# Performance work log

Hardware: AMD Instinct MI355X
Metric: run time of the kernel (lower is better)

The kernel has to match this reference:

```python
import jax, jax.numpy as jnp
import numpy as np

DIM = 768
HEADS = 8
EPS = 1e-6


def _layernorm(x, gamma, beta):
    # torch: mean over last dim; std with Bessel correction (unbiased, ddof=1)
    mean = jnp.mean(x, axis=-1, keepdims=True)
    std = jnp.std(x, axis=-1, keepdims=True, ddof=1)
    return gamma * (x - mean) / (std + EPS) + beta


def setup_inputs() -> dict:
    key = jax.random.key(0)
    ks = jax.random.split(key, 8)
    s = 0.02
    return {
        "x": jax.random.normal(ks[0], (16384, DIM), dtype=jnp.float32),
        "wq_w": jax.random.normal(ks[1], (DIM, DIM), dtype=jnp.float32) * s,
        "wq_b": jnp.zeros((DIM,), dtype=jnp.float32),
        "wk_w": jax.random.normal(ks[2], (DIM, DIM), dtype=jnp.float32) * s,
        "wk_b": jnp.zeros((DIM,), dtype=jnp.float32),
        "wv_w": jax.random.normal(ks[3], (DIM, DIM), dtype=jnp.float32) * s,
        "wv_b": jnp.zeros((DIM,), dtype=jnp.float32),
        "d1_w": jax.random.normal(ks[4], (4 * DIM, DIM), dtype=jnp.float32) * s,
        "d1_b": jnp.zeros((4 * DIM,), dtype=jnp.float32),
        "d2_w": jax.random.normal(ks[5], (DIM, 4 * DIM), dtype=jnp.float32) * s,
        "d2_b": jnp.zeros((DIM,), dtype=jnp.float32),
        "g1": jnp.ones((1,), dtype=jnp.float32),
        "b1": jnp.zeros((1,), dtype=jnp.float32),
        "g2": jnp.ones((1,), dtype=jnp.float32),
        "b2": jnp.zeros((1,), dtype=jnp.float32),
    }


def reference(x, wq_w, wq_b, wk_w, wk_b, wv_w, wv_b,
              d1_w, d1_b, d2_w, d2_b, g1, b1, g2, b2):
    T = x.shape[0]
    # --- pre-LN + attention ---
    xn = _layernorm(x, g1, b1)                      # [T, D]
    q = xn @ wq_w.T + wq_b                          # [T, D]
    k = xn @ wk_w.T + wk_b
    v = xn @ wv_w.T + wv_b
    # faithful to q.view(-1, num_heads, key_dim): groups of HEADS tokens
    q = q.reshape(T // HEADS, HEADS, DIM)
    k = k.reshape(T // HEADS, HEADS, DIM)
    v = v.reshape(T // HEADS, HEADS, DIM)
    scores = jnp.einsum('ghd,gkd->ghk', q, k) / jnp.sqrt(jnp.float32(DIM))
    attn_w = jax.nn.softmax(scores, axis=-1)        # [T/8, 8, 8]
    attn = jnp.einsum('ghk,gkd->ghd', attn_w, v).reshape(T, DIM)
    x = attn + x
    # --- pre-LN + MLP ---
    xn = _layernorm(x, g2, b2)
    h = jax.nn.gelu(xn @ d1_w.T + d1_b, approximate=False)  # [T, 4D]
    x = (h @ d2_w.T + d2_b) + x
    return x
```

## Files before the change

### kernel.cpp

```cpp
#include <hip/hip_runtime.h>
#include <stdint.h>

#define DIM 768
#define HDIM 3072

typedef unsigned short u16;
typedef unsigned char u8;
typedef unsigned int u32;
typedef __bf16 bf16x8 __attribute__((ext_vector_type(8)));
typedef float f32x2 __attribute__((ext_vector_type(2)));
typedef float f32x4 __attribute__((ext_vector_type(4)));
typedef float f32x16 __attribute__((ext_vector_type(16)));
typedef int i32x8 __attribute__((ext_vector_type(8)));

__device__ __forceinline__ u16 f2b(float f) {
    union { float f; unsigned i; } v; v.f = f;
    unsigned r = (v.i + 0x7FFFu + ((v.i >> 16) & 1u)) >> 16;
    return (u16)r;
}
__device__ __forceinline__ unsigned pack2b(float a, float b) {
    return (unsigned)f2b(a) | ((unsigned)f2b(b) << 16);
}
__device__ __forceinline__ float gelu_f(float v) {
    float u = v * (1.5957691216f + 0.07135481627f * v * v);
    float e = __builtin_amdgcn_exp2f(-1.442695041f * u);
    return v * __builtin_amdgcn_rcpf(1.0f + e);
}
__device__ __forceinline__ void gl_lds16(const void* g, void* l) {
    __builtin_amdgcn_global_load_lds(
        (__attribute__((address_space(1))) void*)(g),
        (__attribute__((address_space(3))) void*)(l), 16, 0, 0);
}

__global__ __launch_bounds__(256) void cvt_bf16(const float4* __restrict__ s,
                                                ushort4* __restrict__ d, int n4) {
    int i = blockIdx.x * 256 + threadIdx.x;
    if (i < n4) {
        float4 v = s[i];
        ushort4 o;
        o.x = f2b(v.x); o.y = f2b(v.y); o.z = f2b(v.z); o.w = f2b(v.w);
        d[i] = o;
    }
}

__global__ __launch_bounds__(256) void cvt_fp8(const float4* __restrict__ s,
                                               unsigned* __restrict__ d, int n4) {
    int i = blockIdx.x * 256 + threadIdx.x;
    if (i < n4) {
        float4 v = s[i];
        int p = __builtin_amdgcn_cvt_pk_fp8_f32(v.x, v.y, 0, false);
        p = __builtin_amdgcn_cvt_pk_fp8_f32(v.z, v.w, p, true);
        d[i] = (unsigned)p;
    }
}

__global__ void pack_bias3(const float* __restrict__ a, const float* __restrict__ b,
                           const float* __restrict__ c, float* __restrict__ o) {
    int i = blockIdx.x * 256 + threadIdx.x;
    if (i < DIM) { o[i] = a[i]; o[i + DIM] = b[i]; o[i + 2 * DIM] = c[i]; }
}

__global__ __launch_bounds__(256) void ln_rows_f8(const float* __restrict__ x, u8* __restrict__ xn,
                                                  const float* __restrict__ g, const float* __restrict__ b) {
    int row = blockIdx.x * 4 + (threadIdx.x >> 6);
    int lane = threadIdx.x & 63;
    const float* xr = x + (size_t)row * DIM + lane * 12;
    float v[12];
#pragma unroll
    for (int i = 0; i < 3; ++i) {
        float4 t = ((const float4*)xr)[i];
        v[i * 4 + 0] = t.x; v[i * 4 + 1] = t.y; v[i * 4 + 2] = t.z; v[i * 4 + 3] = t.w;
    }
    float s = 0.f, ss = 0.f;
#pragma unroll
    for (int i = 0; i < 12; ++i) { s += v[i]; ss += v[i] * v[i]; }
#pragma unroll
    for (int o = 32; o; o >>= 1) { s += __shfl_xor(s, o); ss += __shfl_xor(ss, o); }
    float mean = s * (1.f / DIM);
    float var = (ss - (float)DIM * mean * mean) * (1.f / (DIM - 1));
    float denom = sqrtf(var) + 1e-6f;
    float sc = g[0] / denom, bb = b[0] - mean * sc;
    unsigned* outp = (unsigned*)(xn + (size_t)row * DIM + lane * 12);
#pragma unroll
    for (int i = 0; i < 3; ++i) {
        int p = __builtin_amdgcn_cvt_pk_fp8_f32(v[i * 4 + 0] * sc + bb, v[i * 4 + 1] * sc + bb, 0, false);
        p = __builtin_amdgcn_cvt_pk_fp8_f32(v[i * 4 + 2] * sc + bb, v[i * 4 + 3] * sc + bb, p, true);
        outp[i] = (unsigned)p;
    }
}

template <int EPI, int N, int K>
__global__ __launch_bounds__(256)
void gemm_f8(const u8* __restrict__ A, const u8* __restrict__ B,
             const float* __restrict__ bias, const float* __restrict__ resid,
             u8* __restrict__ Co, float* __restrict__ Cf) {
    __shared__ __align__(16) u8 smem[32768];
    u8* As = smem;
    u8* Bs = smem + 16384;
    const int tid = threadIdx.x, lane = tid & 63, wave = tid >> 6;
    const int row0 = blockIdx.x * 128, col0 = blockIdx.y * 128;
    const int wm = (wave >> 1) * 64, wn = (wave & 1) * 64;
    f32x16 acc[2][2] = {};

    const int srow = lane >> 3;
    const int schunk = ((lane & 7) ^ srow) * 16;
    const u8* Ag = A + (size_t)(row0 + wave * 8 + srow) * K + schunk;
    const u8* Bg = B + (size_t)(col0 + wave * 8 + srow) * K + schunk;
    const size_t s32 = (size_t)32 * K;
    u8* AsW = As + wave * 1024;
    u8* BsW = Bs + wave * 1024;

    const int r31 = lane & 31, khalf = lane >> 5;

    for (int kb = 0; kb < K; kb += 128) {
#pragma unroll
        for (int i = 0; i < 4; ++i) {
            gl_lds16(Ag + i * s32, AsW + i * 4096);
            gl_lds16(Bg + i * s32, BsW + i * 4096);
        }
        Ag += 128; Bg += 128;
        __syncthreads();
#pragma unroll
        for (int ks = 0; ks < 2; ++ks) {
            const int c0 = ks * 4 + khalf * 2;
            union { i32x8 v; uint4 q[2]; } af[2], bfr[2];
#pragma unroll
            for (int ib = 0; ib < 2; ++ib) {
                const int r = wm + ib * 32 + r31;
                const u8* base = As + r * 128;
                const int x7 = (r & 7);
                af[ib].q[0] = *(const uint4*)(base + ((c0 ^ x7) * 16));
                af[ib].q[1] = *(const uint4*)(base + (((c0 + 1) ^ x7) * 16));
            }
#pragma unroll
            for (int jb = 0; jb < 2; ++jb) {
                const int r = wn + jb * 32 + r31;
                const u8* base = Bs + r * 128;
                const int x7 = (r & 7);
                bfr[jb].q[0] = *(const uint4*)(base + ((c0 ^ x7) * 16));
                bfr[jb].q[1] = *(const uint4*)(base + (((c0 + 1) ^ x7) * 16));
            }
#pragma unroll
            for (int ib = 0; ib < 2; ++ib)
#pragma unroll
                for (int jb = 0; jb < 2; ++jb)
                    acc[ib][jb] = __builtin_amdgcn_mfma_scale_f32_32x32x64_f8f6f4(
                        bfr[jb].v, af[ib].v, acc[ib][jb], 0, 0,
                        0, 0x7F7F7F7F, 0, 0x7F7F7F7F);
        }
        __syncthreads();
    }
    if (EPI == 0) {
        u32* Cs = (u32*)smem;
#pragma unroll
        for (int ib = 0; ib < 2; ++ib) {
            const int row = wm + ib * 32 + r31;
            const int rx = row & 31;
#pragma unroll
            for (int jb = 0; jb < 2; ++jb)
#pragma unroll
                for (int gq = 0; gq < 4; ++gq) {
                    const int cb = wn + jb * 32 + gq * 8 + 4 * khalf;
                    float4 bv = *(const float4*)(bias + col0 + cb);
                    float v0 = acc[ib][jb][gq * 4 + 0] + bv.x;
                    float v1 = acc[ib][jb][gq * 4 + 1] + bv.y;
                    float v2 = acc[ib][jb][gq * 4 + 2] + bv.z;
                    float v3 = acc[ib][jb][gq * 4 + 3] + bv.w;
                    int p = __builtin_amdgcn_cvt_pk_fp8_f32(v0, v1, 0, false);
                    p = __builtin_amdgcn_cvt_pk_fp8_f32(v2, v3, p, true);
                    Cs[row * 32 + ((cb >> 2) ^ rx)] = (u32)p;
                }
        }
        __syncthreads();
#pragma unroll
        for (int pr = 0; pr < 4; ++pr) {
            const int r = pr * 32 + (tid >> 3);
            const int rx = r & 31;
            const int dwb = (tid & 7) * 4;
            uint4 o;
            o.x = Cs[r * 32 + ((dwb + 0) ^ rx)];
            o.y = Cs[r * 32 + ((dwb + 1) ^ rx)];
            o.z = Cs[r * 32 + ((dwb + 2) ^ rx)];
            o.w = Cs[r * 32 + ((dwb + 3) ^ rx)];
            *(uint4*)(Co + (size_t)(row0 + r) * N + col0 + dwb * 4) = o;
        }
    } else {
        float* Cs = (float*)smem;
#pragma unroll
        for (int pass = 0; pass < 2; ++pass) {
            const int ss = (wm >> 1) + r31;
            const int sx = ss & 7;
#pragma unroll
            for (int jb = 0; jb < 2; ++jb)
#pragma unroll
                for (int gq = 0; gq < 4; ++gq) {
                    const int cb = wn + jb * 32 + gq * 8 + 4 * khalf;
                    float4 bv = *(const float4*)(bias + col0 + cb);
                    float4 v;
                    v.x = acc[pass][jb][gq * 4 + 0] + bv.x;
                    v.y = acc[pass][jb][gq * 4 + 1] + bv.y;
                    v.z = acc[pass][jb][gq * 4 + 2] + bv.z;
                    v.w = acc[pass][jb][gq * 4 + 3] + bv.w;
                    *(float4*)(Cs + ss * 128 + (((cb >> 2) ^ sx) << 2)) = v;
                }
            __syncthreads();
            const int s = tid >> 2;
            const int grow = row0 + (s >> 5) * 64 + pass * 32 + (s & 31);
#pragma unroll
            for (int k = 0; k < 8; ++k) {
                const int c = k * 4 + (tid & 3);
                float4 v = *(const float4*)(Cs + s * 128 + ((c ^ (s & 7)) << 2));
                const size_t gi = (size_t)grow * N + col0 + c * 4;
                float4 rv = *(const float4*)(resid + gi);
                v.x += rv.x; v.y += rv.y; v.z += rv.z; v.w += rv.w;
                *(float4*)(Cf + gi) = v;
            }
            if (pass == 0) __syncthreads();
        }
    }
}

template <int N, int K>
__global__ __launch_bounds__(256)
void gemm_up(const u16* __restrict__ A, const u16* __restrict__ B,
             const float* __restrict__ bias, u8* __restrict__ C8) {
    __shared__ __align__(16) u16 As[128 * 64];
    __shared__ __align__(16) u16 Bs[128 * 64];
    const int tid = threadIdx.x;
    const int row0 = blockIdx.x * 128, col0 = blockIdx.y * 128;
    const int lane = tid & 63, wave = tid >> 6;
    const int wm = (wave >> 1) * 64, wn = (wave & 1) * 64;
    const int la = lane & 15, qd = lane >> 4;
    f32x4 acc[4][4] = {};

    const int srow = lane >> 3;
    const int schunk = (lane & 7) ^ srow;
    const u16* Ag = A + (size_t)(row0 + wave * 8 + srow) * K + schunk * 8;
    const u16* Bg = B + (size_t)(col0 + wave * 8 + srow) * K + schunk * 8;
    const size_t s32 = (size_t)32 * K;
    u16* AsW = &As[wave * 512];
    u16* BsW = &Bs[wave * 512];
    const int x7 = la & 7;

    for (int kb = 0; kb < K; kb += 64) {
#pragma unroll
        for (int i = 0; i < 4; ++i) {
            gl_lds16(Ag + i * s32, AsW + i * 2048);
            gl_lds16(Bg + i * s32, BsW + i * 2048);
        }
        Ag += 64; Bg += 64;
        __syncthreads();
#pragma unroll
        for (int ks = 0; ks < 2; ++ks) {
            const int cp = ((ks * 4 + qd) ^ x7) * 8;
            bf16x8 af[4], bfr[4];
#pragma unroll
            for (int i = 0; i < 4; ++i)
                af[i] = *(const bf16x8*)(&As[(wm + i * 16 + la) * 64 + cp]);
#pragma unroll
            for (int j = 0; j < 4; ++j)
                bfr[j] = *(const bf16x8*)(&Bs[(wn + j * 16 + la) * 64 + cp]);
#pragma unroll
            for (int i = 0; i < 4; ++i)
#pragma unroll
                for (int j = 0; j < 4; ++j)
                    acc[i][j] = __builtin_amdgcn_mfma_f32_16x16x32_bf16(bfr[j], af[i], acc[i][j], 0, 0, 0);
        }
        __syncthreads();
    }
    u32* Cs = (u32*)As;
#pragma unroll
    for (int i = 0; i < 4; ++i) {
        const int row = wm + i * 16 + la;
        const int rx = row & 31;
#pragma unroll
        for (int j = 0; j < 4; ++j) {
            const int cb = wn + j * 16 + qd * 4;
            float4 bv = *(const float4*)(bias + col0 + cb);
            float v0 = gelu_f(acc[i][j][0] + bv.x);
            float v1 = gelu_f(acc[i][j][1] + bv.y);
            float v2 = gelu_f(acc[i][j][2] + bv.z);
            float v3 = gelu_f(acc[i][j][3] + bv.w);
            int p = __builtin_amdgcn_cvt_pk_fp8_f32(v0, v1, 0, false);
            p = __builtin_amdgcn_cvt_pk_fp8_f32(v2, v3, p, true);
            Cs[row * 32 + ((cb >> 2) ^ rx)] = (u32)p;
        }
    }
    __syncthreads();
#pragma unroll
    for (int pr = 0; pr < 4; ++pr) {
        const int r = pr * 32 + (tid >> 3);
        const int rx = r & 31;
        const int dwb = (tid & 7) * 4;
        uint4 o;
        o.x = Cs[r * 32 + ((dwb + 0) ^ rx)];
        o.y = Cs[r * 32 + ((dwb + 1) ^ rx)];
        o.z = Cs[r * 32 + ((dwb + 2) ^ rx)];
        o.w = Cs[r * 32 + ((dwb + 3) ^ rx)];
        *(uint4*)(C8 + (size_t)(row0 + r) * N + col0 + dwb * 4) = o;
    }
}

__global__ __launch_bounds__(256)
void attn_ln(const u8* __restrict__ qkv, const float* __restrict__ x,
             float* __restrict__ x1, u16* __restrict__ xn2,
             const float* __restrict__ g, const float* __restrict__ b) {
    __shared__ __align__(16) u8 sq[8 * 2304];
    __shared__ float sw[64];
    const int tid = threadIdx.x;
    const uint4* src = (const uint4*)(qkv + (size_t)blockIdx.x * (8 * 2304));
    uint4* dst = (uint4*)sq;
#pragma unroll
    for (int i = 0; i < 5; ++i) {
        int idx = tid + i * 256;
        if (idx < 1152) dst[idx] = src[idx];
    }
    __syncthreads();
    const u32* sq32 = (const u32*)sq;
    const int wave = tid >> 6, lane = tid & 63;
#pragma unroll 2
    for (int p = wave * 16; p < wave * 16 + 16; ++p) {
        const u32* qr = sq32 + (p >> 3) * 576 + lane * 3;
        const u32* kr = sq32 + (p & 7) * 576 + 192 + lane * 3;
        float s = 0.f;
#pragma unroll
        for (int i = 0; i < 3; ++i) {
            u32 qd = qr[i], kd = kr[i];
            f32x2 q0 = __builtin_amdgcn_cvt_pk_f32_fp8(qd, false);
            f32x2 q1 = __builtin_amdgcn_cvt_pk_f32_fp8(qd, true);
            f32x2 k0 = __builtin_amdgcn_cvt_pk_f32_fp8(kd, false);
            f32x2 k1 = __builtin_amdgcn_cvt_pk_f32_fp8(kd, true);
            s += q0[0] * k0[0] + q0[1] * k0[1] + q1[0] * k1[0] + q1[1] * k1[1];
        }
#pragma unroll
        for (int o = 32; o; o >>= 1) s += __shfl_xor(s, o);
        if (lane == 0) sw[p] = s;
    }
    __syncthreads();
    if (tid < 8) {
        const float scl = 0.03608439182435161f;
        float e[8]; float m = -1e30f;
#pragma unroll
        for (int j = 0; j < 8; ++j) m = fmaxf(m, sw[tid * 8 + j]);
        float sum = 0.f;
#pragma unroll
        for (int j = 0; j < 8; ++j) { e[j] = expf((sw[tid * 8 + j] - m) * scl); sum += e[j]; }
        float inv = 1.f / sum;
#pragma unroll
        for (int j = 0; j < 8; ++j) sw[tid * 8 + j] = e[j] * inv;
    }
    __syncthreads();
    const int h = tid >> 5, li = tid & 31;
    float w[8];
#pragma unroll
    for (int kk = 0; kk < 8; ++kk) w[kk] = sw[h * 8 + kk];
    const size_t trow = (size_t)blockIdx.x * 8 + h;
    const float* xr = x + trow * DIM;
    float* x1r = x1 + trow * DIM;
    float xv[24], s = 0.f, ss = 0.f;
#pragma unroll
    for (int wd = 0; wd < 3; ++wd) {
        const int d0 = wd * 256 + li * 8;
        float o[8] = {};
#pragma unroll
        for (int kk = 0; kk < 8; ++kk) {
            uint2 vv = *(const uint2*)(sq32 + kk * 576 + 384 + wd * 64 + li * 2);
            f32x2 a0 = __builtin_amdgcn_cvt_pk_f32_fp8(vv.x, false);
            f32x2 a1 = __builtin_amdgcn_cvt_pk_f32_fp8(vv.x, true);
            f32x2 a2 = __builtin_amdgcn_cvt_pk_f32_fp8(vv.y, false);
            f32x2 a3 = __builtin_amdgcn_cvt_pk_f32_fp8(vv.y, true);
            o[0] += w[kk] * a0[0]; o[1] += w[kk] * a0[1];
            o[2] += w[kk] * a1[0]; o[3] += w[kk] * a1[1];
            o[4] += w[kk] * a2[0]; o[5] += w[kk] * a2[1];
            o[6] += w[kk] * a3[0]; o[7] += w[kk] * a3[1];
        }
        float4 xa = *(const float4*)(xr + d0);
        float4 xb = *(const float4*)(xr + d0 + 4);
        float vals[8] = { o[0] + xa.x, o[1] + xa.y, o[2] + xa.z, o[3] + xa.w,
                          o[4] + xb.x, o[5] + xb.y, o[6] + xb.z, o[7] + xb.w };
        float4 w0, w1;
        w0.x = vals[0]; w0.y = vals[1]; w0.z = vals[2]; w0.w = vals[3];
        w1.x = vals[4]; w1.y = vals[5]; w1.z = vals[6]; w1.w = vals[7];
        *(float4*)(x1r + d0) = w0;
        *(float4*)(x1r + d0 + 4) = w1;
#pragma unroll
        for (int e = 0; e < 8; ++e) {
            xv[wd * 8 + e] = vals[e];
            s += vals[e]; ss += vals[e] * vals[e];
        }
    }
#pragma unroll
    for (int o2 = 16; o2; o2 >>= 1) { s += __shfl_xor(s, o2); ss += __shfl_xor(ss, o2); }
    float mean = s * (1.f / 768.f);
    float var = (ss - 768.f * mean * mean) * (1.f / 767.f);
    float denom = sqrtf(var) + 1e-6f;
    float sc = g[0] / denom, bb = b[0] - mean * sc;
    u16* xnr = xn2 + trow * DIM;
#pragma unroll
    for (int wd = 0; wd < 3; ++wd) {
        const int d0 = wd * 256 + li * 8;
        uint4 o;
        o.x = pack2b(xv[wd * 8 + 0] * sc + bb, xv[wd * 8 + 1] * sc + bb);
        o.y = pack2b(xv[wd * 8 + 2] * sc + bb, xv[wd * 8 + 3] * sc + bb);
        o.z = pack2b(xv[wd * 8 + 4] * sc + bb, xv[wd * 8 + 5] * sc + bb);
        o.w = pack2b(xv[wd * 8 + 6] * sc + bb, xv[wd * 8 + 7] * sc + bb);
        *(uint4*)(xnr + d0) = o;
    }
}

extern "C" void kernel_launch(void* const* d_in, const int* in_sizes, int n_in,
                              void* d_out, int out_size, void* d_ws, size_t ws_size,
                              hipStream_t stream) {
    (void)n_in; (void)out_size; (void)ws_size;
    const float* x    = (const float*)d_in[0];
    const float* wq_w = (const float*)d_in[1];
    const float* wq_b = (const float*)d_in[2];
    const float* wk_w = (const float*)d_in[3];
    const float* wk_b = (const float*)d_in[4];
    const float* wv_w = (const float*)d_in[5];
    const float* wv_b = (const float*)d_in[6];
    const float* d1_w = (const float*)d_in[7];
    const float* d1_b = (const float*)d_in[8];
    const float* d2_w = (const float*)d_in[9];
    const float* d2_b = (const float*)d_in[10];
    const float* g1 = (const float*)d_in[11];
    const float* b1 = (const float*)d_in[12];
    const float* g2 = (const float*)d_in[13];
    const float* b2 = (const float*)d_in[14];
    float* out = (float*)d_out;
    char* ws = (char*)d_ws;

    const int T = in_sizes[0] / DIM;

    u8*    w_qkv8 = (u8*)(ws);
    u16*   w_d1   = (u16*)(ws + 1769472);
    u8*    w_d28  = (u8*)(ws + 6488064);
    float* b_qkv  = (float*)(ws + 8847360);
    u16*   xn2    = (u16*)(ws + 8856576);
    float* x1     = (float*)(ws + 34022400);
    u8*    xn1_8  = (u8*)(ws + 34022400);
    u8*    qkv8   = (u8*)(ws + 84354048);
    u8*    h8     = (u8*)(ws + 84354048);

    cvt_fp8<<<576, 256, 0, stream>>>((const float4*)wq_w, (unsigned*)w_qkv8, 147456);
    cvt_fp8<<<576, 256, 0, stream>>>((const float4*)wk_w, (unsigned*)(w_qkv8 + 589824), 147456);
    cvt_fp8<<<576, 256, 0, stream>>>((const float4*)wv_w, (unsigned*)(w_qkv8 + 1179648), 147456);
    cvt_bf16<<<2304, 256, 0, stream>>>((const float4*)d1_w, (ushort4*)w_d1, 589824);
    cvt_fp8<<<2304, 256, 0, stream>>>((const float4*)d2_w, (unsigned*)w_d28, 589824);
    pack_bias3<<<3, 256, 0, stream>>>(wq_b, wk_b, wv_b, b_qkv);

    ln_rows_f8<<<T / 4, 256, 0, stream>>>(x, xn1_8, g1, b1);
    gemm_f8<0, 2304, 768><<<dim3(T / 128, 18), 256, 0, stream>>>(xn1_8, w_qkv8, b_qkv, nullptr, qkv8, nullptr);
    attn_ln<<<T / 8, 256, 0, stream>>>(qkv8, x, x1, xn2, g2, b2);
    gemm_up<3072, 768><<<dim3(T / 128, 24), 256, 0, stream>>>(xn2, w_d1, d1_b, h8);
    gemm_f8<2, 768, 3072><<<dim3(T / 128, 6), 256, 0, stream>>>(h8, w_d28, d2_b, x1, nullptr, out);
}
```

Baseline: 387.7 us.

## Rewrite up-projection GEMM with 256x256 tiles, 512 threads and double-buffered LDS

Result: no change. 387.8 us (+0.0%).

```diff
diff --git a/kernel.cpp b/kernel.cpp
--- a/kernel.cpp
+++ b/kernel.cpp
@@ -221,61 +221,97 @@
 }
 
 template <int N, int K>
-__global__ __launch_bounds__(256)
-void gemm_up(const u16* __restrict__ A, const u16* __restrict__ B,
-             const float* __restrict__ bias, u8* __restrict__ C8) {
-    __shared__ __align__(16) u16 As[128 * 64];
-    __shared__ __align__(16) u16 Bs[128 * 64];
-    const int tid = threadIdx.x;
-    const int row0 = blockIdx.x * 128, col0 = blockIdx.y * 128;
-    const int lane = tid & 63, wave = tid >> 6;
-    const int wm = (wave >> 1) * 64, wn = (wave & 1) * 64;
+__global__ __launch_bounds__(512, 2)
+void gemm_up2(const u16* __restrict__ A, const u16* __restrict__ B,
+              const float* __restrict__ bias, u8* __restrict__ C8) {
+    __shared__ __align__(16) u16 AB[65536];
+    const int tid = threadIdx.x, lane = tid & 63, wave = tid >> 6;
+    const int row0 = blockIdx.x * 256, col0 = blockIdx.y * 256;
+    const int wr = wave >> 2, wc = wave & 3;
     const int la = lane & 15, qd = lane >> 4;
-    f32x4 acc[4][4] = {};
+    f32x4 acc[8][4] = {};
 
     const int srow = lane >> 3;
-    const int schunk = (lane & 7) ^ srow;
-    const u16* Ag = A + (size_t)(row0 + wave * 8 + srow) * K + schunk * 8;
-    const u16* Bg = B + (size_t)(col0 + wave * 8 + srow) * K + schunk * 8;
-    const size_t s32 = (size_t)32 * K;
-    u16* AsW = &As[wave * 512];
-    u16* BsW = &Bs[wave * 512];
-    const int x7 = la & 7;
-
-    for (int kb = 0; kb < K; kb += 64) {
-#pragma unroll
-        for (int i = 0; i < 4; ++i) {
-            gl_lds16(Ag + i * s32, AsW + i * 2048);
-            gl_lds16(Bg + i * s32, BsW + i * 2048);
-        }
-        Ag += 64; Bg += 64;
-        __syncthreads();
-#pragma unroll
-        for (int ks = 0; ks < 2; ++ks) {
-            const int cp = ((ks * 4 + qd) ^ x7) * 8;
-            bf16x8 af[4], bfr[4];
-#pragma unroll
-            for (int i = 0; i < 4; ++i)
-                af[i] = *(const bf16x8*)(&As[(wm + i * 16 + la) * 64 + cp]);
-#pragma unroll
-            for (int j = 0; j < 4; ++j)
-                bfr[j] = *(const bf16x8*)(&Bs[(wn + j * 16 + la) * 64 + cp]);
-#pragma unroll
-            for (int i = 0; i < 4; ++i)
+    const int sc = (lane & 7) ^ srow;
+    const u16* Ag = A + (size_t)(row0 + wave * 8 + srow) * K + sc * 8;
+    const u16* Bg = B + (size_t)(col0 + wave * 8 + srow) * K + sc * 8;
+    const size_t s64r = (size_t)64 * K;
+    u16* AlW = AB + wave * 512;
+    u16* BlW = AB + 32768 + wave * 512;
+    constexpr int NT = K / 64;
+
+#define STAGE_UP(t)                                                         \
+    {                                                                       \
+        const int _b = (t) & 1;                                             \
+        const u16* _ag = Ag + (size_t)(t) * 64;                             \
+        const u16* _bg = Bg + (size_t)(t) * 64;                             \
+        u16* _al = AlW + _b * 16384;                                        \
+        u16* _bl = BlW + _b * 16384;                                        \
+        _Pragma("unroll")                                                   \
+        for (int _i = 0; _i < 4; ++_i) {                                    \
+            gl_lds16(_ag + _i * s64r, _al + _i * 4096);                     \
+            gl_lds16(_bg + _i * s64r, _bl + _i * 4096);                     \
+        }                                                                   \
+    }
+
+    STAGE_UP(0);
+    STAGE_UP(1);
+    asm volatile("s_waitcnt vmcnt(8)" ::: "memory");
+    asm volatile("s_barrier" ::: "memory");
+
+    for (int kt = 0; kt < NT; ++kt) {
+        const u16* Ab = AB + (kt & 1) * 16384;
+        const u16* Bb = AB + 32768 + (kt & 1) * 16384;
+        bf16x8 bf[4][2];
+#pragma unroll
+        for (int j = 0; j < 4; ++j) {
+            const int br = wc * 64 + j * 16 + la;
+            const int bx = br & 7;
+#pragma unroll
+            for (int ks = 0; ks < 2; ++ks)
+                bf[j][ks] = *(const bf16x8*)(Bb + br * 64 + (((ks * 4 + qd) ^ bx) * 8));
+        }
+#pragma unroll
+        for (int q = 0; q < 4; ++q) {
+            bf16x8 af[2][2];
+#pragma unroll
+            for (int ii = 0; ii < 2; ++ii) {
+                const int ar = wr * 128 + (q * 2 + ii) * 16 + la;
+                const int ax = ar & 7;
+#pragma unroll
+                for (int ks = 0; ks < 2; ++ks)
+                    af[ii][ks] = *(const bf16x8*)(Ab + ar * 64 + (((ks * 4 + qd) ^ ax) * 8));
+            }
+            __builtin_amdgcn_s_setprio(1);
+#pragma unroll
+            for (int ii = 0; ii < 2; ++ii)
 #pragma unroll
                 for (int j = 0; j < 4; ++j)
-                    acc[i][j] = __builtin_amdgcn_mfma_f32_16x16x32_bf16(bfr[j], af[i], acc[i][j], 0, 0, 0);
-        }
-        __syncthreads();
-    }
-    u32* Cs = (u32*)As;
-#pragma unroll
-    for (int i = 0; i < 4; ++i) {
-        const int row = wm + i * 16 + la;
-        const int rx = row & 31;
+#pragma unroll
+                    for (int ks = 0; ks < 2; ++ks)
+                        acc[q * 2 + ii][j] = __builtin_amdgcn_mfma_f32_16x16x32_bf16(
+                            bf[j][ks], af[ii][ks], acc[q * 2 + ii][j], 0, 0, 0);
+            __builtin_amdgcn_s_setprio(0);
+        }
+        asm volatile("s_barrier" ::: "memory");
+        if (kt + 2 < NT) {
+            STAGE_UP(kt + 2);
+            asm volatile("s_waitcnt vmcnt(8)" ::: "memory");
+        } else {
+            asm volatile("s_waitcnt vmcnt(0)" ::: "memory");
+        }
+        asm volatile("s_barrier" ::: "memory");
+    }
+#undef STAGE_UP
+
+    u32* Cs = (u32*)AB;
+#pragma unroll
+    for (int i = 0; i < 8; ++i) {
+        const int row = wr * 128 + i * 16 + la;
+        const int rx = row & 63;
 #pragma unroll
         for (int j = 0; j < 4; ++j) {
-            const int cb = wn + j * 16 + qd * 4;
+            const int cb = wc * 64 + j * 16 + qd * 4;
             float4 bv = *(const float4*)(bias + col0 + cb);
             float v0 = gelu_f(acc[i][j][0] + bv.x);
             float v1 = gelu_f(acc[i][j][1] + bv.y);
@@ -283,21 +319,27 @@
             float v3 = gelu_f(acc[i][j][3] + bv.w);
             int p = __builtin_amdgcn_cvt_pk_fp8_f32(v0, v1, 0, false);
             p = __builtin_amdgcn_cvt_pk_fp8_f32(v2, v3, p, true);
-            Cs[row * 32 + ((cb >> 2) ^ rx)] = (u32)p;
+            Cs[row * 64 + ((cb >> 2) ^ rx)] = (u32)p;
         }
     }
     __syncthreads();
 #pragma unroll
     for (int pr = 0; pr < 4; ++pr) {
-        const int r = pr * 32 + (tid >> 3);
-        const int rx = r & 31;
-        const int dwb = (tid & 7) * 4;
-        uint4 o;
-        o.x = Cs[r * 32 + ((dwb + 0) ^ rx)];
-        o.y = Cs[r * 32 + ((dwb + 1) ^ rx)];
-        o.z = Cs[r * 32 + ((dwb + 2) ^ rx)];
-        o.w = Cs[r * 32 + ((dwb + 3) ^ rx)];
-        *(uint4*)(C8 + (size_t)(row0 + r) * N + col0 + dwb * 4) = o;
+        const int r = pr * 64 + (tid >> 3);
+        const int rx = r & 63;
+        const int dwb = (tid & 7) * 8;
+        uint4 o0, o1;
+        o0.x = Cs[r * 64 + ((dwb + 0) ^ rx)];
+        o0.y = Cs[r * 64 + ((dwb + 1) ^ rx)];
+        o0.z = Cs[r * 64 + ((dwb + 2) ^ rx)];
+        o0.w = Cs[r * 64 + ((dwb + 3) ^ rx)];
+        o1.x = Cs[r * 64 + ((dwb + 4) ^ rx)];
+        o1.y = Cs[r * 64 + ((dwb + 5) ^ rx)];
+        o1.z = Cs[r * 64 + ((dwb + 6) ^ rx)];
+        o1.w = Cs[r * 64 + ((dwb + 7) ^ rx)];
+        u8* outp = C8 + (size_t)(row0 + r) * N + col0 + dwb * 4;
+        *(uint4*)(outp) = o0;
+        *(uint4*)(outp + 16) = o1;
     }
 }
 
@@ -452,6 +494,6 @@
     ln_rows_f8<<<T / 4, 256, 0, stream>>>(x, xn1_8, g1, b1);
     gemm_f8<0, 2304, 768><<<dim3(T / 128, 18), 256, 0, stream>>>(xn1_8, w_qkv8, b_qkv, nullptr, qkv8, nullptr);
     attn_ln<<<T / 8, 256, 0, stream>>>(qkv8, x, x1, xn2, g2, b2);
-    gemm_up<3072, 768><<<dim3(T / 128, 24), 256, 0, stream>>>(xn2, w_d1, d1_b, h8);
+    gemm_up2<3072, 768><<<dim3(T / 256, 12), 512, 0, stream>>>(xn2, w_d1, d1_b, h8);
     gemm_f8<2, 768, 3072><<<dim3(T / 128, 6), 256, 0, stream>>>(h8, w_d28, d2_b, x1, nullptr, out);
 }
```
